# Kernel tuning notes

Hardware: AMD Instinct MI355X
Metric: run time of the kernel (lower is better)

Reference implementation:

```python
import jax, jax.numpy as jnp
import numpy as np

B, T, D = 2, 2048, 1024
H, DH = 16, 64  # heads, head_dim; inner_dim = H*DH = D
EPS = 1e-6


def _rmsnorm(x, g):
    # torch.nn.RMSNorm over last dim with affine weight g
    return x * jax.lax.rsqrt(jnp.mean(x * x, axis=-1, keepdims=True) + EPS) * g


def _interleaved_rope(x, cos, sin):
    # x: [B, T, D]; pairs (x0, x1) rotated: rot = [-x1, x0, -x3, x2, ...]
    b, t, d = x.shape
    x2 = x.reshape(b, t, d // 2, 2)
    rot = jnp.stack([-x2[..., 1], x2[..., 0]], axis=-1).reshape(b, t, d)
    return x * cos + rot * sin


def setup_inputs() -> dict:
    key = jax.random.key(0)
    ks = jax.random.split(key, 8)
    hidden_states = jax.random.normal(ks[0], (B, T, D), dtype=jnp.float32)
    cos = jax.random.uniform(ks[1], (1, T, D), dtype=jnp.float32)
    sin = jax.random.uniform(ks[2], (1, T, D), dtype=jnp.float32)
    s = 0.02  # init scale for weights
    wq = jax.random.normal(ks[3], (D, D), dtype=jnp.float32) * s
    wk = jax.random.normal(ks[4], (D, D), dtype=jnp.float32) * s
    wv = jax.random.normal(ks[5], (D, D), dtype=jnp.float32) * s
    wo = jax.random.normal(ks[6], (D, D), dtype=jnp.float32) * s
    bq = jnp.zeros((D,), jnp.float32)
    bk = jnp.zeros((D,), jnp.float32)
    bv = jnp.zeros((D,), jnp.float32)
    bo = jnp.zeros((D,), jnp.float32)
    gq = jnp.ones((D,), jnp.float32)
    gk = jnp.ones((D,), jnp.float32)
    return {
        'hidden_states': hidden_states, 'cos': cos, 'sin': sin,
        'wq': wq, 'bq': bq, 'wk': wk, 'bk': bk, 'wv': wv, 'bv': bv,
        'gq': gq, 'gk': gk, 'wo': wo, 'bo': bo,
    }


def reference(hidden_states, cos, sin, wq, bq, wk, bk, wv, bv, gq, gk, wo, bo):
    # QKV projections (weights stored as [in, out]) + RMSNorm(q,k) + RoPE
    q = _interleaved_rope(_rmsnorm(hidden_states @ wq + bq, gq), cos, sin)
    k = _interleaved_rope(_rmsnorm(hidden_states @ wk + bk, gk), cos, sin)
    v = hidden_states @ wv + bv

    # split heads: [B, T, D] -> [B, H, T, DH]
    def split(x):
        return x.reshape(B, T, H, DH).transpose(0, 2, 1, 3)
    q, k, v = split(q), split(k), split(v)

    scale = 1.0 / jnp.sqrt(jnp.float32(DH))
    scores = jnp.einsum('bhqd,bhkd->bhqk', q, k) * scale
    attn = jax.nn.softmax(scores, axis=-1)
    out = jnp.einsum('bhqk,bhkd->bhqd', attn, v)

    # merge heads + output projection
    out = out.transpose(0, 2, 1, 3).reshape(B, T, D)
    return out @ wo + bo
```

## Files before the change

### kernel.cpp

```cpp
#include <hip/hip_runtime.h>

typedef _Float16 f16;
typedef _Float16 f16x8 __attribute__((ext_vector_type(8)));
typedef _Float16 f16x4 __attribute__((ext_vector_type(4)));
typedef _Float16 f16x2 __attribute__((ext_vector_type(2)));
typedef float f32x4 __attribute__((ext_vector_type(4)));

#define MFMA(a, b, c) __builtin_amdgcn_mfma_f32_16x16x32_f16(a, b, c, 0, 0, 0)
#define PKRTZ(a, b) __builtin_bit_cast(f16x2, __builtin_amdgcn_cvt_pkrtz(a, b))

__device__ __forceinline__ void gload16(const void* g, void* l) {
  __builtin_amdgcn_global_load_lds((const __attribute__((address_space(1))) char*)g,
                                   (__attribute__((address_space(3))) char*)l, 16, 0, 0);
}


__global__ __launch_bounds__(256) void k_cvt_hidden(const float* __restrict__ x, f16* __restrict__ y) {
  int i = blockIdx.x * 256 + threadIdx.x;
  float4 v = ((const float4*)x)[i];
  f16x4 h; h[0] = (f16)v.x; h[1] = (f16)v.y; h[2] = (f16)v.z; h[3] = (f16)v.w;
  ((f16x4*)y)[i] = h;
}

__global__ __launch_bounds__(256) void k_cvt_w(const float* __restrict__ w0, const float* __restrict__ w1,
                                               const float* __restrict__ w2, const float* __restrict__ w3,
                                               f16* __restrict__ wt) {
  int z = blockIdx.z;
  const float* w = z == 0 ? w0 : z == 1 ? w1 : z == 2 ? w2 : w3;
  f16* dst = wt + (size_t)z * 1024 * 1024;
  __shared__ float tile[64][65];
  int t = threadIdx.x;
  int k0 = blockIdx.x * 64, n0 = blockIdx.y * 64;
  int cr = t >> 4, cc = (t & 15) * 4;
#pragma unroll
  for (int p = 0; p < 4; p++) {
    int r = cr + p * 16;
    float4 v = *(const float4*)&w[(size_t)(k0 + r) * 1024 + n0 + cc];
    tile[r][cc + 0] = v.x; tile[r][cc + 1] = v.y; tile[r][cc + 2] = v.z; tile[r][cc + 3] = v.w;
  }
  __syncthreads();
#pragma unroll
  for (int p = 0; p < 4; p++) {
    int nn = cr + p * 16;
    f16x4 h;
    h[0] = (f16)tile[cc + 0][nn]; h[1] = (f16)tile[cc + 1][nn];
    h[2] = (f16)tile[cc + 2][nn]; h[3] = (f16)tile[cc + 3][nn];
    *(f16x4*)&dst[(size_t)(n0 + nn) * 1024 + k0 + cc] = h;
  }
}

template <bool OUTF32>
__device__ __forceinline__ void gemm_core(const f16* __restrict__ A, const f16* __restrict__ W,
                                          const float* __restrict__ bias,
                                          f16* __restrict__ oh, float* __restrict__ of) {
  __shared__ f16 Al[128 * 64];
  __shared__ f16 Bl[128 * 64];
  const int t = threadIdx.x;
  const int lane = t & 63, wid = t >> 6;
  const int lr = lane & 15, lg = lane >> 4;
  const int m0 = blockIdx.x * 128, n0 = blockIdx.y * 128;
  const int wm = wid >> 1, wn = wid & 1;
  const int lrow = lane >> 3;
  const int cb = (((lane & 7) ^ lrow) << 4);

  f32x4 acc[4][4] = {};

  for (int k0 = 0; k0 < 1024; k0 += 64) {
    __syncthreads();
#pragma unroll
    for (int it = 0; it < 4; it++) {
      int rbase = it * 32 + wid * 8;
      int row = rbase + lrow;
      gload16((const char*)&A[(size_t)(m0 + row) * 1024 + k0] + cb, (char*)Al + rbase * 128);
      gload16((const char*)&W[(size_t)(n0 + row) * 1024 + k0] + cb, (char*)Bl + rbase * 128);
    }
    __syncthreads();
    f16x8 af[2][4], bf[2][4];
#pragma unroll
    for (int x = 0; x < 4; x++) {
      int ra = wm * 64 + x * 16 + lr;
      int rb = wn * 64 + x * 16 + lr;
#pragma unroll
      for (int kh = 0; kh < 2; kh++) {
        int ca = (kh * 64 + lg * 16) ^ ((lr & 7) << 4);
        af[kh][x] = *(const f16x8*)((char*)Al + ra * 128 + ca);
        bf[kh][x] = *(const f16x8*)((char*)Bl + rb * 128 + ca);
      }
    }
#pragma unroll
    for (int kh = 0; kh < 2; kh++)
#pragma unroll
      for (int mt = 0; mt < 4; mt++)
#pragma unroll
        for (int nt = 0; nt < 4; nt++)
          acc[mt][nt] = MFMA(af[kh][mt], bf[kh][nt], acc[mt][nt]);
  }
#pragma unroll
  for (int mt = 0; mt < 4; mt++) {
#pragma unroll
    for (int nt = 0; nt < 4; nt++) {
      int col = n0 + wn * 64 + nt * 16 + lr;
      float bcol = bias[col];
#pragma unroll
      for (int e = 0; e < 4; e++) {
        int row = m0 + wm * 64 + mt * 16 + lg * 4 + e;
        float val = acc[mt][nt][e] + bcol;
        if (OUTF32) of[(size_t)row * 1024 + col] = val;
        else        oh[(size_t)row * 1024 + col] = (f16)val;
      }
    }
  }
}

__global__ __launch_bounds__(256, 2) void k_gemm_qkv(const f16* __restrict__ A, const f16* __restrict__ wt,
                                                     const float* __restrict__ bq, const float* __restrict__ bk,
                                                     const float* __restrict__ bv,
                                                     f16* __restrict__ q, f16* __restrict__ k, f16* __restrict__ v) {
  int z = blockIdx.z;
  gemm_core<false>(A, wt + (size_t)z * 1024 * 1024,
                   z == 0 ? bq : z == 1 ? bk : bv,
                   z == 0 ? q : z == 1 ? k : v, nullptr);
}

__global__ __launch_bounds__(256, 2) void k_gemm_o(const f16* __restrict__ A, const f16* __restrict__ wt,
                                                   const float* __restrict__ bo, float* __restrict__ out) {
  gemm_core<true>(A, wt, bo, nullptr, out);
}

__global__ __launch_bounds__(256) void k_normrope(f16* __restrict__ qh, f16* __restrict__ kh,
                                                  const float* __restrict__ gq, const float* __restrict__ gk,
                                                  const float* __restrict__ cs, const float* __restrict__ sn) {
  int row = blockIdx.x, which = blockIdx.y;
  f16* buf = which ? kh : qh;
  const float* g = which ? gk : gq;
  int t = threadIdx.x, c4 = t * 4;
  f16x4 xv = *(const f16x4*)&buf[(size_t)row * 1024 + c4];
  float x0 = xv[0], x1 = xv[1], x2 = xv[2], x3 = xv[3];
  float ss = x0 * x0 + x1 * x1 + x2 * x2 + x3 * x3;
#pragma unroll
  for (int off = 1; off < 64; off <<= 1) ss += __shfl_xor(ss, off);
  __shared__ float red[4];
  if ((t & 63) == 0) red[t >> 6] = ss;
  __syncthreads();
  float inv = rsqrtf((red[0] + red[1] + red[2] + red[3]) * (1.0f / 1024.0f) + 1e-6f);
  int tt = row & 2047;
  float4 cv = *(const float4*)&cs[(size_t)tt * 1024 + c4];
  float4 sv = *(const float4*)&sn[(size_t)tt * 1024 + c4];
  float4 gv = *(const float4*)&g[c4];
  float y0 = x0 * inv * gv.x, y1 = x1 * inv * gv.y, y2 = x2 * inv * gv.z, y3 = x3 * inv * gv.w;
  f16x4 ov;
  ov[0] = (f16)(y0 * cv.x - y1 * sv.x);
  ov[1] = (f16)(y1 * cv.y + y0 * sv.y);
  ov[2] = (f16)(y2 * cv.z - y3 * sv.z);
  ov[3] = (f16)(y3 * cv.w + y2 * sv.w);
  *(f16x4*)&buf[(size_t)row * 1024 + c4] = ov;
}

__global__ __launch_bounds__(256) void k_vtrans(const f16* __restrict__ vh, f16* __restrict__ vt) {
  __shared__ f16 tile[64][65];
  int t = threadIdx.x;
  int t0 = blockIdx.x * 64;
  int bh = blockIdx.y;
  int b = bh >> 4, h = bh & 15;
  int rr = t >> 3, c8 = (t & 7) * 8;
#pragma unroll
  for (int p = 0; p < 2; p++) {
    int r = p * 32 + rr;
    f16x8 v = *(const f16x8*)&vh[(size_t)(b * 2048 + t0 + r) * 1024 + h * 64 + c8];
#pragma unroll
    for (int j = 0; j < 8; j++) tile[r][c8 + j] = v[j];
  }
  __syncthreads();
#pragma unroll
  for (int p = 0; p < 2; p++) {
    int dh = p * 32 + rr;
    f16x8 o;
#pragma unroll
    for (int j = 0; j < 8; j++) o[j] = tile[c8 + j][dh];
    *(f16x8*)&vt[((size_t)bh * 64 + dh) * 2048 + t0 + c8] = o;
  }
}

#define ASWZ(row) ((((row) & 3) | (((row) & 8) >> 1)) << 4)

__global__ __launch_bounds__(256, 4) void k_attn(const f16* __restrict__ qh, const f16* __restrict__ kh,
                                                 const f16* __restrict__ vt, f16* __restrict__ ao) {
  __shared__ f16 Kl[2][64 * 64];
  __shared__ f16 Vl[2][64 * 64];
  const int t = threadIdx.x;
  const int lane = t & 63, wid = t >> 6;
  const int lr = lane & 15, lg = lane >> 4;
  const int lgb = lg << 4;
  const int raw = blockIdx.y * 32 + blockIdx.x;
  const int mybh = ((raw & 7) << 2) | ((raw >> 3) & 3);
  const int myq = raw >> 5;
  const int b = mybh >> 4, h = mybh & 15;
  const int q0 = myq * 64 + wid * 16;
  const f16* Qb = qh + ((size_t)(b * 2048 + q0)) * 1024 + h * 64;
  f16x8 qf0 = *(const f16x8*)&Qb[(size_t)lr * 1024 + lg * 8];
  f16x8 qf1 = *(const f16x8*)&Qb[(size_t)lr * 1024 + 32 + lg * 8];
  const f16* Kg = kh + ((size_t)b * 2048) * 1024 + h * 64;
  const f16* Vg = vt + ((size_t)mybh) * 64 * 2048;
  const int lrow = lane >> 3;
  const int sg = (lane & 7) << 4;
  const float sc = 0.125f * 1.44269504088896340736f;
  float m = -1e30f, l = 0.f;
  f32x4 acc[4] = {};

  auto stage = [&](int kvo, int bs) {
#pragma unroll
    for (int i = 0; i < 2; i++) {
      int rbase = (i * 4 + wid) * 8;
      int row = rbase + lrow;
      int cswz = sg ^ ASWZ(row);
      gload16((const char*)(Kg + (size_t)(kvo + row) * 1024) + cswz, (char*)&Kl[bs][0] + rbase * 128);
      gload16((const char*)(Vg + (size_t)row * 2048 + kvo) + cswz, (char*)&Vl[bs][0] + rbase * 128);
    }
  };

  stage(0, 0);
  __syncthreads();
  int cur = 0;

  for (int kv0 = 0; kv0 < 2048; kv0 += 64) {
    if (kv0 + 64 < 2048) stage(kv0 + 64, cur ^ 1);
    const char* Kb = (const char*)&Kl[cur][0];
    const char* Vb = (const char*)&Vl[cur][0];

    f32x4 s[4];
#pragma unroll
    for (int ks = 0; ks < 4; ks++) {
      int key = ((lr >> 2) << 3) + (lr & 3) + ((ks & 1) << 2) + ((ks >> 1) << 5);
      int sw = ASWZ(key);
      f16x8 kf0 = *(const f16x8*)(Kb + key * 128 + (lgb ^ sw));
      f16x8 kf1 = *(const f16x8*)(Kb + key * 128 + ((64 + lgb) ^ sw));
      f32x4 z = {};
      z = MFMA(kf0, qf0, z);
      z = MFMA(kf1, qf1, z);
      s[ks] = z;
    }

    float smax = fmaxf(fmaxf(s[0][0], s[0][1]), s[0][2]);
    smax = fmaxf(fmaxf(smax, s[0][3]), s[1][0]);
    smax = fmaxf(fmaxf(smax, s[1][1]), s[1][2]);
    smax = fmaxf(fmaxf(smax, s[1][3]), s[2][0]);
    smax = fmaxf(fmaxf(smax, s[2][1]), s[2][2]);
    smax = fmaxf(fmaxf(smax, s[2][3]), s[3][0]);
    smax = fmaxf(fmaxf(smax, s[3][1]), s[3][2]);
    smax = fmaxf(smax, s[3][3]);
    smax = fmaxf(smax, __shfl_xor(smax, 16));
    smax = fmaxf(smax, __shfl_xor(smax, 32));
    float smc = smax * sc;

    if (!__all(smc - m <= 8.f)) {
      float mn = fmaxf(m, smc);
      float al = exp2f(m - mn);
      m = mn;
      float alq[4];
#pragma unroll
      for (int e = 0; e < 4; e++) alq[e] = __shfl(al, lg * 4 + e);
      l *= al;
#pragma unroll
      for (int ds = 0; ds < 4; ds++)
#pragma unroll
        for (int e = 0; e < 4; e++) acc[ds][e] *= alq[e];
    }

    float sum = 0.f;
    union { f16x8 v; f16x2 h[4]; } u[2];
#pragma unroll
    for (int ks = 0; ks < 4; ks++) {
      float p0 = exp2f(fmaf(s[ks][0], sc, -m));
      float p1 = exp2f(fmaf(s[ks][1], sc, -m));
      float p2 = exp2f(fmaf(s[ks][2], sc, -m));
      float p3 = exp2f(fmaf(s[ks][3], sc, -m));
      sum += (p0 + p1) + (p2 + p3);
      u[ks >> 1].h[(ks & 1) * 2 + 0] = PKRTZ(p0, p1);
      u[ks >> 1].h[(ks & 1) * 2 + 1] = PKRTZ(p2, p3);
    }
    sum += __shfl_xor(sum, 16);
    sum += __shfl_xor(sum, 32);
    l += sum;

#pragma unroll
    for (int ds = 0; ds < 4; ds++) {
      int vrow = ds * 16 + lr;
      int sw = ASWZ(vrow);
      f16x8 vf0 = *(const f16x8*)(Vb + vrow * 128 + (lgb ^ sw));
      f16x8 vf1 = *(const f16x8*)(Vb + vrow * 128 + ((64 + lgb) ^ sw));
      acc[ds] = MFMA(u[0].v, vf0, acc[ds]);
      acc[ds] = MFMA(u[1].v, vf1, acc[ds]);
    }

    __syncthreads();
    cur ^= 1;
  }

  float lf[4];
#pragma unroll
  for (int e = 0; e < 4; e++) lf[e] = 1.f / __shfl(l, lg * 4 + e);
#pragma unroll
  for (int e = 0; e < 4; e++) {
    size_t row = (size_t)(b * 2048 + q0 + lg * 4 + e);
#pragma unroll
    for (int ds = 0; ds < 4; ds++)
      ao[row * 1024 + h * 64 + ds * 16 + lr] = (f16)(acc[ds][e] * lf[e]);
  }
}

extern "C" void kernel_launch(void* const* d_in, const int* in_sizes, int n_in,
                              void* d_out, int out_size, void* d_ws, size_t ws_size,
                              hipStream_t stream) {
  const float* hid  = (const float*)d_in[0];
  const float* cosb = (const float*)d_in[1];
  const float* sinb = (const float*)d_in[2];
  const float* wq = (const float*)d_in[3];
  const float* bq = (const float*)d_in[4];
  const float* wk = (const float*)d_in[5];
  const float* bk = (const float*)d_in[6];
  const float* wv = (const float*)d_in[7];
  const float* bv = (const float*)d_in[8];
  const float* gq = (const float*)d_in[9];
  const float* gk = (const float*)d_in[10];
  const float* wo = (const float*)d_in[11];
  const float* bo = (const float*)d_in[12];
  float* out = (float*)d_out;

  char* ws = (char*)d_ws;
  f16* aH  = (f16*)(ws);
  f16* wt  = (f16*)(ws + ((size_t)8 << 20));
  f16* qh  = (f16*)(ws + ((size_t)16 << 20));
  f16* khb = (f16*)(ws + ((size_t)24 << 20));
  f16* vhb = (f16*)(ws + ((size_t)32 << 20));
  f16* vtb = (f16*)(ws + ((size_t)40 << 20));
  f16* ao  = (f16*)(ws + ((size_t)48 << 20));

  k_cvt_hidden<<<dim3(4096), dim3(256), 0, stream>>>(hid, aH);
  k_cvt_w<<<dim3(16, 16, 4), dim3(256), 0, stream>>>(wq, wk, wv, wo, wt);
  k_gemm_qkv<<<dim3(32, 8, 3), dim3(256), 0, stream>>>(aH, wt, bq, bk, bv, qh, khb, vhb);
  k_normrope<<<dim3(4096, 2), dim3(256), 0, stream>>>(qh, khb, gq, gk, cosb, sinb);
  k_vtrans<<<dim3(32, 32), dim3(256), 0, stream>>>(vhb, vtb);
  k_attn<<<dim3(32, 32), dim3(256), 0, stream>>>(qh, khb, vtb, ao);
  k_gemm_o<<<dim3(32, 8, 1), dim3(256), 0, stream>>>(ao, wt + (size_t)3 * 1024 * 1024, bo, out);
}
```

Measured before the change: 154.9 us.

## Double-buffer GEMM LDS, widen attention to 32 rows per wave, MFMA row sums

The GEMM core now double-buffers its A/B LDS tiles, prefetching the next K slice while computing the current one, and raises wave priority around the MFMA blocks. The QKV GEMM is flattened into a 2D grid where blockIdx.y selects which of q, k or v a block writes. The attention kernel processes two 16-row query groups per wave (128 queries per block, 512 blocks), reusing each K/V fragment across both groups, and computes the softmax denominators with an extra MFMA against a ones vector instead of shuffle reductions. Occupancy hints drop to 2 blocks per CU for attention, and the doubled LDS and extra registers may reduce residency.

```diff
diff --git a/kernel.cpp b/kernel.cpp
--- a/kernel.cpp
+++ b/kernel.cpp
@@ -50,31 +50,35 @@
 }
 
 template <bool OUTF32>
-__device__ __forceinline__ void gemm_core(const f16* __restrict__ A, const f16* __restrict__ W,
-                                          const float* __restrict__ bias,
+__device__ __forceinline__ void gemm_core(const f16* __restrict__ A, const f16* __restrict__ Wrows,
+                                          const float* __restrict__ bias, int m0,
                                           f16* __restrict__ oh, float* __restrict__ of) {
-  __shared__ f16 Al[128 * 64];
-  __shared__ f16 Bl[128 * 64];
+  __shared__ f16 Al[2][128 * 64];
+  __shared__ f16 Bl[2][128 * 64];
   const int t = threadIdx.x;
   const int lane = t & 63, wid = t >> 6;
   const int lr = lane & 15, lg = lane >> 4;
-  const int m0 = blockIdx.x * 128, n0 = blockIdx.y * 128;
   const int wm = wid >> 1, wn = wid & 1;
   const int lrow = lane >> 3;
   const int cb = (((lane & 7) ^ lrow) << 4);
 
   f32x4 acc[4][4] = {};
 
-  for (int k0 = 0; k0 < 1024; k0 += 64) {
-    __syncthreads();
+  auto stage = [&](int k0, int bs) {
 #pragma unroll
     for (int it = 0; it < 4; it++) {
       int rbase = it * 32 + wid * 8;
       int row = rbase + lrow;
-      gload16((const char*)&A[(size_t)(m0 + row) * 1024 + k0] + cb, (char*)Al + rbase * 128);
-      gload16((const char*)&W[(size_t)(n0 + row) * 1024 + k0] + cb, (char*)Bl + rbase * 128);
-    }
-    __syncthreads();
+      gload16((const char*)&A[(size_t)(m0 + row) * 1024 + k0] + cb, (char*)&Al[bs][0] + rbase * 128);
+      gload16((const char*)&Wrows[(size_t)row * 1024 + k0] + cb, (char*)&Bl[bs][0] + rbase * 128);
+    }
+  };
+
+  stage(0, 0);
+  __syncthreads();
+  int cur = 0;
+  for (int k0 = 0; k0 < 1024; k0 += 64) {
+    if (k0 + 64 < 1024) stage(k0 + 64, cur ^ 1);
     f16x8 af[2][4], bf[2][4];
 #pragma unroll
     for (int x = 0; x < 4; x++) {
@@ -83,10 +87,11 @@
 #pragma unroll
       for (int kh = 0; kh < 2; kh++) {
         int ca = (kh * 64 + lg * 16) ^ ((lr & 7) << 4);
-        af[kh][x] = *(const f16x8*)((char*)Al + ra * 128 + ca);
-        bf[kh][x] = *(const f16x8*)((char*)Bl + rb * 128 + ca);
-      }
-    }
+        af[kh][x] = *(const f16x8*)((char*)&Al[cur][0] + ra * 128 + ca);
+        bf[kh][x] = *(const f16x8*)((char*)&Bl[cur][0] + rb * 128 + ca);
+      }
+    }
+    __builtin_amdgcn_s_setprio(1);
 #pragma unroll
     for (int kh = 0; kh < 2; kh++)
 #pragma unroll
@@ -94,12 +99,15 @@
 #pragma unroll
         for (int nt = 0; nt < 4; nt++)
           acc[mt][nt] = MFMA(af[kh][mt], bf[kh][nt], acc[mt][nt]);
+    __builtin_amdgcn_s_setprio(0);
+    __syncthreads();
+    cur ^= 1;
   }
 #pragma unroll
   for (int mt = 0; mt < 4; mt++) {
 #pragma unroll
     for (int nt = 0; nt < 4; nt++) {
-      int col = n0 + wn * 64 + nt * 16 + lr;
+      int col = wn * 64 + nt * 16 + lr;
       float bcol = bias[col];
 #pragma unroll
       for (int e = 0; e < 4; e++) {
@@ -116,15 +124,17 @@
                                                      const float* __restrict__ bq, const float* __restrict__ bk,
                                                      const float* __restrict__ bv,
                                                      f16* __restrict__ q, f16* __restrict__ k, f16* __restrict__ v) {
-  int z = blockIdx.z;
-  gemm_core<false>(A, wt + (size_t)z * 1024 * 1024,
-                   z == 0 ? bq : z == 1 ? bk : bv,
-                   z == 0 ? q : z == 1 ? k : v, nullptr);
-}
-
-__global__ __launch_bounds__(256, 2) void k_gemm_o(const f16* __restrict__ A, const f16* __restrict__ wt,
+  int n0 = blockIdx.y * 128;
+  int zsel = n0 >> 10, cbs = n0 & 1023;
+  const float* bias = (zsel == 0 ? bq : zsel == 1 ? bk : bv) + cbs;
+  f16* dst = (zsel == 0 ? q : zsel == 1 ? k : v) + cbs;
+  gemm_core<false>(A, wt + (size_t)n0 * 1024, bias, blockIdx.x * 128, dst, nullptr);
+}
+
+__global__ __launch_bounds__(256, 2) void k_gemm_o(const f16* __restrict__ A, const f16* __restrict__ wt3,
                                                    const float* __restrict__ bo, float* __restrict__ out) {
-  gemm_core<true>(A, wt, bo, nullptr, out);
+  int n0 = blockIdx.y * 128;
+  gemm_core<true>(A, wt3 + (size_t)n0 * 1024, bo + n0, blockIdx.x * 128, nullptr, out + n0);
 }
 
 __global__ __launch_bounds__(256) void k_normrope(f16* __restrict__ qh, f16* __restrict__ kh,
@@ -183,7 +193,7 @@
 
 #define ASWZ(row) ((((row) & 3) | (((row) & 8) >> 1)) << 4)
 
-__global__ __launch_bounds__(256, 4) void k_attn(const f16* __restrict__ qh, const f16* __restrict__ kh,
+__global__ __launch_bounds__(256, 2) void k_attn(const f16* __restrict__ qh, const f16* __restrict__ kh,
                                                  const f16* __restrict__ vt, f16* __restrict__ ao) {
   __shared__ f16 Kl[2][64 * 64];
   __shared__ f16 Vl[2][64 * 64];
@@ -191,21 +201,28 @@
   const int lane = t & 63, wid = t >> 6;
   const int lr = lane & 15, lg = lane >> 4;
   const int lgb = lg << 4;
-  const int raw = blockIdx.y * 32 + blockIdx.x;
+  const int raw = blockIdx.x;
   const int mybh = ((raw & 7) << 2) | ((raw >> 3) & 3);
   const int myq = raw >> 5;
   const int b = mybh >> 4, h = mybh & 15;
-  const int q0 = myq * 64 + wid * 16;
+  const int q0 = myq * 128 + wid * 32;
   const f16* Qb = qh + ((size_t)(b * 2048 + q0)) * 1024 + h * 64;
-  f16x8 qf0 = *(const f16x8*)&Qb[(size_t)lr * 1024 + lg * 8];
-  f16x8 qf1 = *(const f16x8*)&Qb[(size_t)lr * 1024 + 32 + lg * 8];
+  f16x8 qf[2][2];
+#pragma unroll
+  for (int g = 0; g < 2; g++) {
+    qf[g][0] = *(const f16x8*)&Qb[(size_t)(g * 16 + lr) * 1024 + lg * 8];
+    qf[g][1] = *(const f16x8*)&Qb[(size_t)(g * 16 + lr) * 1024 + 32 + lg * 8];
+  }
   const f16* Kg = kh + ((size_t)b * 2048) * 1024 + h * 64;
   const f16* Vg = vt + ((size_t)mybh) * 64 * 2048;
   const int lrow = lane >> 3;
   const int sg = (lane & 7) << 4;
   const float sc = 0.125f * 1.44269504088896340736f;
-  float m = -1e30f, l = 0.f;
-  f32x4 acc[4] = {};
+  float m[2] = {-1e30f, -1e30f};
+  f32x4 acc[2][4] = {};
+  f32x4 accl[2] = {};
+  const f16 ov1 = (lr == 0) ? (f16)1.0f : (f16)0.0f;
+  const f16x8 onesf = {ov1, ov1, ov1, ov1, ov1, ov1, ov1, ov1};
 
   auto stage = [&](int kvo, int bs) {
 #pragma unroll
@@ -227,84 +244,99 @@
     const char* Kb = (const char*)&Kl[cur][0];
     const char* Vb = (const char*)&Vl[cur][0];
 
-    f32x4 s[4];
+    f32x4 s[2][4];
+    __builtin_amdgcn_s_setprio(1);
 #pragma unroll
     for (int ks = 0; ks < 4; ks++) {
       int key = ((lr >> 2) << 3) + (lr & 3) + ((ks & 1) << 2) + ((ks >> 1) << 5);
       int sw = ASWZ(key);
       f16x8 kf0 = *(const f16x8*)(Kb + key * 128 + (lgb ^ sw));
       f16x8 kf1 = *(const f16x8*)(Kb + key * 128 + ((64 + lgb) ^ sw));
-      f32x4 z = {};
-      z = MFMA(kf0, qf0, z);
-      z = MFMA(kf1, qf1, z);
-      s[ks] = z;
-    }
-
-    float smax = fmaxf(fmaxf(s[0][0], s[0][1]), s[0][2]);
-    smax = fmaxf(fmaxf(smax, s[0][3]), s[1][0]);
-    smax = fmaxf(fmaxf(smax, s[1][1]), s[1][2]);
-    smax = fmaxf(fmaxf(smax, s[1][3]), s[2][0]);
-    smax = fmaxf(fmaxf(smax, s[2][1]), s[2][2]);
-    smax = fmaxf(fmaxf(smax, s[2][3]), s[3][0]);
-    smax = fmaxf(fmaxf(smax, s[3][1]), s[3][2]);
-    smax = fmaxf(smax, s[3][3]);
-    smax = fmaxf(smax, __shfl_xor(smax, 16));
-    smax = fmaxf(smax, __shfl_xor(smax, 32));
-    float smc = smax * sc;
-
-    if (!__all(smc - m <= 8.f)) {
-      float mn = fmaxf(m, smc);
-      float al = exp2f(m - mn);
-      m = mn;
-      float alq[4];
-#pragma unroll
-      for (int e = 0; e < 4; e++) alq[e] = __shfl(al, lg * 4 + e);
-      l *= al;
-#pragma unroll
-      for (int ds = 0; ds < 4; ds++)
-#pragma unroll
-        for (int e = 0; e < 4; e++) acc[ds][e] *= alq[e];
-    }
-
-    float sum = 0.f;
-    union { f16x8 v; f16x2 h[4]; } u[2];
-#pragma unroll
-    for (int ks = 0; ks < 4; ks++) {
-      float p0 = exp2f(fmaf(s[ks][0], sc, -m));
-      float p1 = exp2f(fmaf(s[ks][1], sc, -m));
-      float p2 = exp2f(fmaf(s[ks][2], sc, -m));
-      float p3 = exp2f(fmaf(s[ks][3], sc, -m));
-      sum += (p0 + p1) + (p2 + p3);
-      u[ks >> 1].h[(ks & 1) * 2 + 0] = PKRTZ(p0, p1);
-      u[ks >> 1].h[(ks & 1) * 2 + 1] = PKRTZ(p2, p3);
-    }
-    sum += __shfl_xor(sum, 16);
-    sum += __shfl_xor(sum, 32);
-    l += sum;
-
+#pragma unroll
+      for (int g = 0; g < 2; g++) {
+        f32x4 z = {};
+        z = MFMA(kf0, qf[g][0], z);
+        z = MFMA(kf1, qf[g][1], z);
+        s[g][ks] = z;
+      }
+    }
+    __builtin_amdgcn_s_setprio(0);
+
+    union U { f16x8 v; f16x2 h[4]; } u[2][2];
+#pragma unroll
+    for (int g = 0; g < 2; g++) {
+      float smax = fmaxf(fmaxf(s[g][0][0], s[g][0][1]), s[g][0][2]);
+      smax = fmaxf(fmaxf(smax, s[g][0][3]), s[g][1][0]);
+      smax = fmaxf(fmaxf(smax, s[g][1][1]), s[g][1][2]);
+      smax = fmaxf(fmaxf(smax, s[g][1][3]), s[g][2][0]);
+      smax = fmaxf(fmaxf(smax, s[g][2][1]), s[g][2][2]);
+      smax = fmaxf(fmaxf(smax, s[g][2][3]), s[g][3][0]);
+      smax = fmaxf(fmaxf(smax, s[g][3][1]), s[g][3][2]);
+      smax = fmaxf(smax, s[g][3][3]);
+      smax = fmaxf(smax, __shfl_xor(smax, 16));
+      smax = fmaxf(smax, __shfl_xor(smax, 32));
+      float smc = smax * sc;
+
+      if (!__all(smc - m[g] <= 8.f)) {
+        float mn = fmaxf(m[g], smc);
+        float al = exp2f(m[g] - mn);
+        m[g] = mn;
+        float alq[4];
+#pragma unroll
+        for (int e = 0; e < 4; e++) alq[e] = __shfl(al, lg * 4 + e);
+#pragma unroll
+        for (int ds = 0; ds < 4; ds++)
+#pragma unroll
+          for (int e = 0; e < 4; e++) acc[g][ds][e] *= alq[e];
+#pragma unroll
+        for (int e = 0; e < 4; e++) accl[g][e] *= alq[e];
+      }
+
+#pragma unroll
+      for (int ks = 0; ks < 4; ks++) {
+        float p0 = exp2f(fmaf(s[g][ks][0], sc, -m[g]));
+        float p1 = exp2f(fmaf(s[g][ks][1], sc, -m[g]));
+        float p2 = exp2f(fmaf(s[g][ks][2], sc, -m[g]));
+        float p3 = exp2f(fmaf(s[g][ks][3], sc, -m[g]));
+        u[g][ks >> 1].h[(ks & 1) * 2 + 0] = PKRTZ(p0, p1);
+        u[g][ks >> 1].h[(ks & 1) * 2 + 1] = PKRTZ(p2, p3);
+      }
+    }
+
+    __builtin_amdgcn_s_setprio(1);
 #pragma unroll
     for (int ds = 0; ds < 4; ds++) {
       int vrow = ds * 16 + lr;
       int sw = ASWZ(vrow);
       f16x8 vf0 = *(const f16x8*)(Vb + vrow * 128 + (lgb ^ sw));
       f16x8 vf1 = *(const f16x8*)(Vb + vrow * 128 + ((64 + lgb) ^ sw));
-      acc[ds] = MFMA(u[0].v, vf0, acc[ds]);
-      acc[ds] = MFMA(u[1].v, vf1, acc[ds]);
-    }
+#pragma unroll
+      for (int g = 0; g < 2; g++) {
+        acc[g][ds] = MFMA(u[g][0].v, vf0, acc[g][ds]);
+        acc[g][ds] = MFMA(u[g][1].v, vf1, acc[g][ds]);
+      }
+    }
+#pragma unroll
+    for (int g = 0; g < 2; g++) {
+      accl[g] = MFMA(u[g][0].v, onesf, accl[g]);
+      accl[g] = MFMA(u[g][1].v, onesf, accl[g]);
+    }
+    __builtin_amdgcn_s_setprio(0);
 
     __syncthreads();
     cur ^= 1;
   }
 
-  float lf[4];
-#pragma unroll
-  for (int e = 0; e < 4; e++) lf[e] = 1.f / __shfl(l, lg * 4 + e);
-#pragma unroll
-  for (int e = 0; e < 4; e++) {
-    size_t row = (size_t)(b * 2048 + q0 + lg * 4 + e);
-#pragma unroll
-    for (int ds = 0; ds < 4; ds++)
-      ao[row * 1024 + h * 64 + ds * 16 + lr] = (f16)(acc[ds][e] * lf[e]);
+#pragma unroll
+  for (int g = 0; g < 2; g++) {
+#pragma unroll
+    for (int e = 0; e < 4; e++) {
+      float lf = 1.f / __shfl(accl[g][e], lg << 4);
+      size_t row = (size_t)(b * 2048 + q0 + g * 16 + lg * 4 + e);
+#pragma unroll
+      for (int ds = 0; ds < 4; ds++)
+        ao[row * 1024 + h * 64 + ds * 16 + lr] = (f16)(acc[g][ds][e] * lf);
+    }
   }
 }
 
@@ -337,9 +369,9 @@
 
   k_cvt_hidden<<<dim3(4096), dim3(256), 0, stream>>>(hid, aH);
   k_cvt_w<<<dim3(16, 16, 4), dim3(256), 0, stream>>>(wq, wk, wv, wo, wt);
-  k_gemm_qkv<<<dim3(32, 8, 3), dim3(256), 0, stream>>>(aH, wt, bq, bk, bv, qh, khb, vhb);
+  k_gemm_qkv<<<dim3(32, 24), dim3(256), 0, stream>>>(aH, wt, bq, bk, bv, qh, khb, vhb);
   k_normrope<<<dim3(4096, 2), dim3(256), 0, stream>>>(qh, khb, gq, gk, cosb, sinb);
   k_vtrans<<<dim3(32, 32), dim3(256), 0, stream>>>(vhb, vtb);
-  k_attn<<<dim3(32, 32), dim3(256), 0, stream>>>(qh, khb, vtb, ao);
-  k_gemm_o<<<dim3(32, 8, 1), dim3(256), 0, stream>>>(ao, wt + (size_t)3 * 1024 * 1024, bo, out);
-}
+  k_attn<<<dim3(512), dim3(256), 0, stream>>>(qh, khb, vtb, ao);
+  k_gemm_o<<<dim3(32, 8), dim3(256), 0, stream>>>(ao, wt + (size_t)3 * 1024 * 1024, bo, out);
+}
```

Result: faster. 143.2 us (-7.5%).
